# Kernel optimization log

Measured on AMD Instinct MI355X. Metric: run time of the kernel, lower is better.

Reference implementation:

```python
import jax, jax.numpy as jnp
import numpy as np

B, N, V, C, H, W = 4, 2048, 4, 64, 32, 32
D, K, OUT, HEADS = 128, 64, 256, 4
IMG_W, IMG_H = W * 14.0, H * 14.0
EPS_NORM = 1e-12


def setup_inputs() -> dict:
    key = jax.random.key(0)
    ks = iter(jax.random.split(key, 64))
    nk = lambda: next(ks)
    rn = lambda shape, s=1.0: jax.random.normal(nk(), shape, jnp.float32) * s
    eye4 = jnp.broadcast_to(jnp.eye(4, dtype=jnp.float32), (B, V, 4, 4))
    Kbase = jnp.array([[400.0, 0.0, IMG_W / 2], [0.0, 400.0, IMG_H / 2], [0.0, 0.0, 1.0]], jnp.float32)
    inp = {
        'gaussians': rn((B, N, 14)),
        'visual_feats': rn((B * V, C, H, W)),
        'extrinsics': eye4 + rn((B, V, 4, 4), 0.1),
        'intrinsics': jnp.broadcast_to(Kbase, (B, V, 3, 3)) + rn((B, V, 3, 3), 0.5),
        'offsets': rn((B, N, 2), 0.05),
        'pg_w': rn((D, 14), 0.1), 'pg_b': jnp.zeros((D,)), 'pg_ln_g': jnp.ones((D,)), 'pg_ln_b': jnp.zeros((D,)),
        'pv_w': rn((D, C), 0.1), 'pv_b': jnp.zeros((D,)), 'pv_ln_g': jnp.ones((D,)), 'pv_ln_b': jnp.zeros((D,)),
        'attn_ipw': rn((2, 3 * D, D), 0.05), 'attn_ipb': jnp.zeros((2, 3 * D)),
        'attn_ow': rn((2, D, D), 0.05), 'attn_ob': jnp.zeros((2, D)),
        'dca_ln_g': jnp.ones((2, D)), 'dca_ln_b': jnp.zeros((2, D)),
        'gate_w': rn((D, 2 * D), 0.05), 'gate_b': jnp.zeros((D,)),
        'router_w1': rn((D, 2 * D), 0.05), 'router_b1': jnp.zeros((D,)),
        'router_ln_g': jnp.ones((D,)), 'router_ln_b': jnp.zeros((D,)),
        'router_w2': rn((3, D), 0.01), 'router_b2': jnp.array([-3.0, -3.0, 2.0], jnp.float32),
        'vlad_cent': jnp.clip(rn((3, K, D), 0.01), -2.0, 2.0),
        'vlad_cw': rn((3, K, D), 0.05), 'vlad_cb': jnp.zeros((3, K)),
        'bn_w': rn((3, OUT, K * D), 0.01), 'bn_b': jnp.zeros((3, OUT)),
        'bn_ln_g': jnp.ones((3, OUT)), 'bn_ln_b': jnp.zeros((3, OUT)),
    }
    return inp


def _ln(x, g, b, eps=1e-5):
    m = x.mean(-1, keepdims=True)
    v = ((x - m) ** 2).mean(-1, keepdims=True)
    return (x - m) * jax.lax.rsqrt(v + eps) * g + b


def _l2n(x, axis):
    return x / jnp.maximum(jnp.linalg.norm(x, axis=axis, keepdims=True), EPS_NORM)


def _bilinear(fm, grid):
    # fm: [BV,H,W,C]; grid: [BV,N,2] in [-1,1]; align_corners=False, zero padding
    x = (grid[..., 0] + 1.0) * 0.5 * W - 0.5
    y = (grid[..., 1] + 1.0) * 0.5 * H - 0.5
    x0, y0 = jnp.floor(x), jnp.floor(y)
    fmf = fm.reshape(fm.shape[0], H * W, C)
    out = jnp.zeros((fm.shape[0], grid.shape[1], C), jnp.float32)
    for xi in (x0, x0 + 1.0):
        for yi in (y0, y0 + 1.0):
            wgt = (1.0 - jnp.abs(x - xi)) * (1.0 - jnp.abs(y - yi))
            valid = (xi >= 0) & (xi < W) & (yi >= 0) & (yi < H)
            idx = (jnp.clip(yi, 0, H - 1) * W + jnp.clip(xi, 0, W - 1)).astype(jnp.int32)
            v = jnp.take_along_axis(fmf, idx[..., None], axis=1)
            out = out + v * (wgt * valid.astype(jnp.float32))[..., None]
    return out


def _mha(q, k, v, ipw, ipb, ow, ob):
    Wq, Wk, Wv = jnp.split(ipw, 3, axis=0)
    bq, bk, bv = jnp.split(ipb, 3)
    dh = D // HEADS
    sh = lambda x, Wt, b: (x @ Wt.T + b).reshape(x.shape[0], x.shape[1], HEADS, dh)
    qh, kh, vh = sh(q, Wq, bq), sh(k, Wk, bk), sh(v, Wv, bv)
    att = jax.nn.softmax(jnp.einsum('bqhd,bkhd->bhqk', qh, kh) * (1.0 / np.sqrt(dh)), axis=-1)
    o = jnp.einsum('bhqk,bkhd->bqhd', att, vh).reshape(q.shape[0], q.shape[1], D)
    return o @ ow.T + ob


def _netvlad(x, cent, cw, cb):
    xn = _l2n(x, 2)                                   # [B,N,D]
    a = jax.nn.softmax(xn @ cw.T + cb, axis=-1)       # [B,N,K]
    # sum_n a[bnk]*(x[bnd]-c[kd]) without materializing [B,N,K,D]
    vlad = jnp.einsum('bnk,bnd->bkd', a, xn) - a.sum(1)[..., None] * cent
    vlad = _l2n(vlad, 2).reshape(x.shape[0], -1)
    return _l2n(vlad, 1)


def reference(gaussians, visual_feats, extrinsics, intrinsics, offsets,
              pg_w, pg_b, pg_ln_g, pg_ln_b, pv_w, pv_b, pv_ln_g, pv_ln_b,
              attn_ipw, attn_ipb, attn_ow, attn_ob, dca_ln_g, dca_ln_b,
              gate_w, gate_b, router_w1, router_b1, router_ln_g, router_ln_b,
              router_w2, router_b2, vlad_cent, vlad_cw, vlad_cb,
              bn_w, bn_b, bn_ln_g, bn_ln_b):
    # ---- DynamicProjectionLayer (vectorized over views) ----
    ph = jnp.concatenate([gaussians[:, :, :3], jnp.ones((B, N, 1), jnp.float32)], axis=2)
    cam = jnp.einsum('bvij,bnj->bvni', extrinsics, ph)          # [B,V,N,4]
    p2h = jnp.einsum('bvij,bvnj->bvni', intrinsics, cam[..., :3])
    depth = jnp.maximum(p2h[..., 2:3], 1e-6)
    p2 = p2h[..., :2] / depth
    grid = 2.0 * p2 / jnp.array([IMG_W, IMG_H], jnp.float32) - 1.0 + offsets[:, None]
    fm = visual_feats.reshape(B, V, C, H, W).transpose(0, 1, 3, 4, 2).reshape(B * V, H, W, C)
    sampled = _bilinear(fm, grid.reshape(B * V, N, 2)).reshape(B, V, N, C)
    valid = ((depth[..., 0] > 0.1) & (grid[..., 0] >= -1) & (grid[..., 0] <= 1)
             & (grid[..., 1] >= -1) & (grid[..., 1] <= 1)).astype(jnp.float32)[..., None]
    vfeat = (sampled * valid).sum(1) / (valid.sum(1) + 1e-8)     # [B,N,C]
    # ---- GaussianEncoder ----
    g_emb = jax.nn.relu(_ln(gaussians @ pg_w.T + pg_b, pg_ln_g, pg_ln_b))
    v_emb = jax.nn.relu(_ln(vfeat @ pv_w.T + pv_b, pv_ln_g, pv_ln_b))
    f_g2v = _ln(g_emb + _mha(g_emb, v_emb, v_emb, attn_ipw[0], attn_ipb[0], attn_ow[0], attn_ob[0]),
                dca_ln_g[0], dca_ln_b[0])
    f_v2g = _ln(v_emb + _mha(v_emb, g_emb, g_emb, attn_ipw[1], attn_ipb[1], attn_ow[1], attn_ob[1]),
                dca_ln_g[1], dca_ln_b[1])
    gate = jax.nn.sigmoid(jnp.concatenate([f_g2v, f_v2g], -1) @ gate_w.T + gate_b)
    fused = f_g2v * gate + f_v2g * (1.0 - gate)
    ri = jnp.concatenate([g_emb.mean(1), v_emb.mean(1)], -1)
    rw = jax.nn.softmax(jax.nn.relu(_ln(ri @ router_w1.T + router_b1, router_ln_g, router_ln_b))
                        @ router_w2.T + router_b2, axis=-1)
    descs = []
    for i, feat in enumerate((g_emb, v_emb, fused)):
        d = _netvlad(feat, vlad_cent[i], vlad_cw[i], vlad_cb[i])
        d = _ln(d @ bn_w[i].T + bn_b[i], bn_ln_g[i], bn_ln_b[i])
        descs.append(_l2n(d, 1))
    final = rw[:, 0:1] * descs[0] + rw[:, 1:2] * descs[1] + rw[:, 2:3] * descs[2]
    return _l2n(final, 1), rw
```

## Files before the change

kernel.cpp:

```cpp
#include <hip/hip_runtime.h>
#include <math.h>

typedef float f32x4 __attribute__((ext_vector_type(4)));
typedef short s16x8 __attribute__((ext_vector_type(8)));

#define DEV static __device__ __forceinline__

DEV float wsum(float v){
  #pragma unroll
  for(int m=1;m<64;m<<=1) v += __shfl_xor(v,m);
  return v;
}
template<int NW>
DEV float bsum(float v, float* s){
  v = wsum(v);
  int w = threadIdx.x>>6;
  if((threadIdx.x&63)==0) s[w]=v;
  __syncthreads();
  float r = 0.f;
  #pragma unroll
  for(int i=0;i<NW;++i) r += s[i];
  __syncthreads();
  return r;
}
DEV float xexp2(float x){
#if __has_builtin(__builtin_amdgcn_exp2f)
  return __builtin_amdgcn_exp2f(x);
#else
  return exp2f(x);
#endif
}
DEV unsigned pkbf(float lo, float hi){
  unsigned r;
  asm("v_cvt_pk_bf16_f32 %0, %1, %2" : "=v"(r) : "v"(lo), "v"(hi));
  return r;
}
DEV unsigned short bf16c(float v){ return (unsigned short)(pkbf(v, 0.f) & 0xffffu); }
DEV float ubf_lo(unsigned u){ unsigned b=(u&0xffffu)<<16; return __builtin_bit_cast(float,b); }
DEV float ubf_hi(unsigned u){ unsigned b=(u>>16)<<16;    return __builtin_bit_cast(float,b); }
union FR { unsigned u[4]; s16x8 v; uint4 q; };

DEV f32x4 MF(s16x8 a, s16x8 b, f32x4 c){
  return __builtin_amdgcn_mfma_f32_16x16x32_bf16(a, b, c, 0,0,0);
}

DEV void gl_lds16(const void* g, void* l){
  __builtin_amdgcn_global_load_lds(
    (const __attribute__((address_space(1))) void*)g,
    (__attribute__((address_space(3))) void*)l, 16, 0, 0);
}

__global__ __launch_bounds__(256) void k_trfm(const float* __restrict__ vf, float* __restrict__ fmT){
  int hc = blockIdx.x, bv = blockIdx.y, t = threadIdx.x;
  __shared__ float ts[64][65];
  const float* src = vf + (size_t)bv*65536 + hc*64;
  int c = t>>2, q = t&3;
  #pragma unroll
  for(int i=0;i<4;++i){
    float4 v4 = *(const float4*)(src + (size_t)c*1024 + q*16 + i*4);
    ts[c][q*16+i*4+0]=v4.x; ts[c][q*16+i*4+1]=v4.y;
    ts[c][q*16+i*4+2]=v4.z; ts[c][q*16+i*4+3]=v4.w;
  }
  __syncthreads();
  int hw = t>>2;
  float* dst = fmT + ((size_t)bv*1024 + hc*64 + hw)*64 + q*16;
  #pragma unroll
  for(int i=0;i<4;++i){
    int cb = q*16 + i*4;
    float4 o4;
    o4.x = ts[cb+0][hw]; o4.y = ts[cb+1][hw]; o4.z = ts[cb+2][hw]; o4.w = ts[cb+3][hw];
    *(float4*)(dst + i*4) = o4;
  }
}

__global__ __launch_bounds__(256) void k_proj(const float* __restrict__ gs, const float* __restrict__ fmT,
                       const float* __restrict__ E, const float* __restrict__ Kin,
                       const float* __restrict__ off, float* __restrict__ vfeat){
  int bn = blockIdx.x*4 + (threadIdx.x>>6); int b = bn>>11; int c = threadIdx.x&63;
  const float* g = gs + (size_t)bn*14;
  float px = g[0], py = g[1], pz = g[2];
  float ox = off[bn*2+0], oy = off[bn*2+1];
  float acc = 0.f, vsum = 0.f;
  for(int v=0; v<4; ++v){
    const float* e = E + ((b*4+v)*16);
    float cx = e[0]*px + e[1]*py + e[2]*pz + e[3];
    float cy = e[4]*px + e[5]*py + e[6]*pz + e[7];
    float cz = e[8]*px + e[9]*py + e[10]*pz + e[11];
    const float* kk = Kin + ((b*4+v)*9);
    float ux = kk[0]*cx + kk[1]*cy + kk[2]*cz;
    float uy = kk[3]*cx + kk[4]*cy + kk[5]*cz;
    float uz = kk[6]*cx + kk[7]*cy + kk[8]*cz;
    float dep = fmaxf(uz, 1e-6f);
    float gx = 2.f*(ux/dep)*(1.f/448.f) - 1.f + ox;
    float gy = 2.f*(uy/dep)*(1.f/448.f) - 1.f + oy;
    float valid = (uz > 0.1f && gx >= -1.f && gx <= 1.f && gy >= -1.f && gy <= 1.f) ? 1.f : 0.f;
    float x = (gx+1.f)*16.f - 0.5f;
    float y = (gy+1.f)*16.f - 0.5f;
    float x0 = floorf(x), y0 = floorf(y);
    const float* fbase = fmT + (size_t)(b*4+v)*65536 + c;
    float sv = 0.f;
    #pragma unroll
    for(int t=0;t<4;++t){
      float xi = x0 + (float)(t&1), yi = y0 + (float)(t>>1);
      float wgt = (1.f - fabsf(x-xi))*(1.f - fabsf(y-yi));
      bool vt = (xi>=0.f && xi<32.f && yi>=0.f && yi<32.f);
      int xc = (int)fminf(fmaxf(xi,0.f),31.f);
      int yc = (int)fminf(fmaxf(yi,0.f),31.f);
      float smp = fbase[(yc*32+xc)*64];
      sv += vt ? wgt*smp : 0.f;
    }
    acc += valid * sv;
    vsum += valid;
  }
  vfeat[(size_t)bn*64 + c] = acc / (vsum + 1e-8f);
}

__global__ void k_embed(const float* __restrict__ gs, const float* __restrict__ vfeat,
   const float* __restrict__ pg_w, const float* __restrict__ pg_b,
   const float* __restrict__ pg_g, const float* __restrict__ pg_bb,
   const float* __restrict__ pv_w, const float* __restrict__ pv_b,
   const float* __restrict__ pv_g, const float* __restrict__ pv_bb,
   float* __restrict__ gemb, float* __restrict__ vemb,
   unsigned short* __restrict__ gembb, unsigned short* __restrict__ vembb){
  __shared__ float xs[64]; __shared__ float gsr[14]; __shared__ float red[2];
  int row = blockIdx.x; int d = threadIdx.x;
  if(d<14) gsr[d] = gs[(size_t)row*14+d];
  if(d<64) xs[d] = vfeat[(size_t)row*64+d];
  __syncthreads();
  float a = pg_b[d];
  #pragma unroll
  for(int j=0;j<14;++j) a += gsr[j]*pg_w[d*14+j];
  float mu = bsum<2>(a, red)*(1.f/128.f);
  float df = a-mu;
  float var = bsum<2>(df*df, red)*(1.f/128.f);
  float y = fmaxf(df*rsqrtf(var+1e-5f)*pg_g[d] + pg_bb[d], 0.f);
  gemb[(size_t)row*128+d] = y;
  gembb[(size_t)row*128+d] = bf16c(y);
  float av = pv_b[d];
  #pragma unroll
  for(int j=0;j<64;++j) av += xs[j]*pv_w[d*64+j];
  mu = bsum<2>(av, red)*(1.f/128.f);
  df = av-mu;
  var = bsum<2>(df*df, red)*(1.f/128.f);
  y = fmaxf(df*rsqrtf(var+1e-5f)*pv_g[d] + pv_bb[d], 0.f);
  vemb[(size_t)row*128+d] = y;
  vembb[(size_t)row*128+d] = bf16c(y);
}

__global__ void k_wprep(const float* __restrict__ ipw, const float* __restrict__ ow,
                        const float* __restrict__ gw, const float* __restrict__ cw,
                        unsigned short* __restrict__ WB){
  int i = blockIdx.x*256 + threadIdx.x;
  if(i >= 188416) return;
  float v;
  if(i < 98304)       v = ipw[i];
  else if(i < 131072) v = ow[i-98304];
  else if(i < 163840) v = gw[i-131072];
  else                v = cw[i-163840];
  WB[i] = bf16c(v);
}

__global__ __launch_bounds__(256) void k_qkv(const unsigned short* __restrict__ GEb,
    const unsigned short* __restrict__ VEb, const unsigned short* __restrict__ WB,
    const float* __restrict__ ipb, unsigned* __restrict__ QKVu, float qsc){
  int mt = blockIdx.x, y = blockIdx.y;
  int m = y/6, j6 = y%6, kind = j6>>1, n0 = (j6&1)*64;
  const unsigned short* A = (kind==0) ? (m?VEb:GEb) : (m?GEb:VEb);
  const unsigned short* W = WB + m*49152 + kind*16384;
  const float* bias = ipb + m*384 + kind*128;
  unsigned* outb = QKVu + (size_t)m*1572864 + (size_t)kind*524288;
  float scale = (kind==0)? qsc : 1.f;
  int m0 = mt*64;
  int wid=threadIdx.x>>6, lane=threadIdx.x&63, lr=lane&15, lg=lane>>4;
  const unsigned short* ap = A + (size_t)(m0+wid*16+lr)*128 + lg*8;
  f32x4 acc[4] = {{0,0,0,0},{0,0,0,0},{0,0,0,0},{0,0,0,0}};
  #pragma unroll
  for(int ks=0; ks<128; ks+=32){
    FR af; af.v = *(const s16x8*)(ap + ks);
    #pragma unroll
    for(int nt=0; nt<4; ++nt){
      FR bf; bf.v = *(const s16x8*)(W + (size_t)(n0+nt*16+lr)*128 + ks + lg*8);
      acc[nt] = MF(af.v, bf.v, acc[nt]);
    }
  }
  __shared__ float xs[64][65];
  #pragma unroll
  for(int nt=0; nt<4; ++nt){
    float bv = bias[n0+nt*16+lr];
    #pragma unroll
    for(int r=0;r<4;++r) xs[wid*16+lg*4+r][nt*16+lr] = (acc[nt][r]+bv)*scale;
  }
  __syncthreads();
  if(kind<2){
    int i = threadIdx.x>>2, s = threadIdx.x&3;
    int gr = m0 + i, b = gr>>11, nn = gr&2047;
    int j0 = n0 + s*16, h = j0>>5, d0 = j0&31;
    unsigned w[8];
    #pragma unroll
    for(int p=0;p<8;++p) w[p] = pkbf(xs[i][s*16+2*p], xs[i][s*16+2*p+1]);
    unsigned* dst = outb + ((size_t)(b*4+h)*2048+nn)*16 + (d0>>1);
    uint4 u0; u0.x=w[0];u0.y=w[1];u0.z=w[2];u0.w=w[3];
    uint4 u1; u1.x=w[4];u1.y=w[5];u1.z=w[6];u1.w=w[7];
    *(uint4*)dst = u0; *(uint4*)(dst+4) = u1;
  } else {
    int c = threadIdx.x>>2, rs = threadIdx.x&3;
    int j = n0 + c, h = j>>5, d = j&31;
    int b = m0>>11, nn0 = m0&2047;
    unsigned w[8];
    #pragma unroll
    for(int p=0;p<8;++p) w[p] = pkbf(xs[rs*16+2*p][c], xs[rs*16+2*p+1][c]);
    unsigned* dst = outb + (size_t)(b*4+h)*32768 + (size_t)d*1024 + ((nn0+rs*16)>>1);
    uint4 u0; u0.x=w[0];u0.y=w[1];u0.z=w[2];u0.w=w[3];
    uint4 u1; u1.x=w[4];u1.y=w[5];u1.z=w[6];u1.w=w[7];
    *(uint4*)dst = u0; *(uint4*)(dst+4) = u1;
  }
}

__global__ __launch_bounds__(256) void k_flash(const unsigned short* __restrict__ QKV,
    unsigned* __restrict__ OPARTw, float* __restrict__ LSUM){
  int qt = blockIdx.x, h = blockIdx.y, z = blockIdx.z;
  int mb = z&7, split = z>>3;
  int m = mb>>2, b = mb&3;
  const unsigned short* base = QKV + (size_t)m*3145728;
  const unsigned short* qp = base + (size_t)(b*4+h)*65536;
  const unsigned short* kp = qp + 1048576;
  const unsigned short* vp = qp + 2097152;
  int tid=threadIdx.x, wid=tid>>6, lane=tid&63, lr=lane&15, lg=lane>>4;
  __shared__ unsigned short KT[2][2048];
  __shared__ unsigned short VT[2][2048];
  __shared__ unsigned Ps[4][16][33];
  int q0 = qt*64 + wid*16;
  int kbase = split*1024;
  FR qf; qf.v = *(const s16x8*)(qp + (size_t)(q0+lr)*32 + lg*8);
  const f32x4 zz = {0.f,0.f,0.f,0.f};
  f32x4 o0g = zz, o1g = zz;
  float lrun = 0.f;
  unsigned* prow = &Ps[wid][lr][0];
  int kr = wid*16 + (lane>>2);
  int kscol = (((lane&3)<<3) ^ (((lane>>3)&3)<<3));
  const unsigned short* ksrc0 = kp + (size_t)(kbase + kr)*32 + kscol;
  int vrow = wid*8 + (lane>>3);
  int vscol = 8*((lane&7) ^ (lane>>3));
  const unsigned short* vsrc0 = vp + (size_t)vrow*2048 + kbase + vscol;
  int kkey = ((lr>>1)&3)<<3;
  int ko = lr*32 + ((lg*8) ^ kkey);
  int sw = (lr&7)*8;
  int vo0 = lr*64 + ((lg*8) ^ sw);
  int vo2 = lr*64 + ((32+lg*8) ^ sw);
  gl_lds16(ksrc0, &KT[0][wid*512]);
  gl_lds16(vsrc0, &VT[0][wid*512]);
  __syncthreads();
  int buf = 0;
  for(int t=0; t<16; ++t){
    int tn = (t+1)&15;
    gl_lds16(ksrc0 + (size_t)tn*2048, &KT[buf^1][wid*512]);
    gl_lds16(vsrc0 + tn*64,           &VT[buf^1][wid*512]);
    const unsigned short* Ktb = &KT[buf][0];
    const unsigned short* Vtb = &VT[buf][0];
    FR k0,k1,k2,k3;
    k0.v = *(const s16x8*)(Ktb + ko);
    k1.v = *(const s16x8*)(Ktb +  512 + ko);
    k2.v = *(const s16x8*)(Ktb + 1024 + ko);
    k3.v = *(const s16x8*)(Ktb + 1536 + ko);
    f32x4 s0 = MF(k0.v, qf.v, zz);
    f32x4 s1 = MF(k1.v, qf.v, zz);
    f32x4 s2 = MF(k2.v, qf.v, zz);
    f32x4 s3 = MF(k3.v, qf.v, zz);
    float p0[4],p1[4],p2[4],p3[4]; float ps=0.f;
    #pragma unroll
    for(int r=0;r<4;++r){
      p0[r]=xexp2(s0[r]); p1[r]=xexp2(s1[r]);
      p2[r]=xexp2(s2[r]); p3[r]=xexp2(s3[r]);
      ps += p0[r]+p1[r]+p2[r]+p3[r];
    }
    lrun += ps;
    asm volatile("" ::: "memory");
    prow[   lg*2+0]=pkbf(p0[0],p0[1]); prow[   lg*2+1]=pkbf(p0[2],p0[3]);
    prow[ 8+lg*2+0]=pkbf(p1[0],p1[1]); prow[ 8+lg*2+1]=pkbf(p1[2],p1[3]);
    prow[16+lg*2+0]=pkbf(p2[0],p2[1]); prow[16+lg*2+1]=pkbf(p2[2],p2[3]);
    prow[24+lg*2+0]=pkbf(p3[0],p3[1]); prow[24+lg*2+1]=pkbf(p3[2],p3[3]);
    asm volatile("" ::: "memory");
    FR pf0, pf1;
    #pragma unroll
    for(int i=0;i<4;++i){ pf0.u[i]=prow[lg*4+i]; pf1.u[i]=prow[16+lg*4+i]; }
    FR v0,v1,v2,v3;
    v0.v = *(const s16x8*)(Vtb + vo0);
    v1.v = *(const s16x8*)(Vtb + 1024 + vo0);
    v2.v = *(const s16x8*)(Vtb + vo2);
    v3.v = *(const s16x8*)(Vtb + 1024 + vo2);
    o0g = MF(v0.v, pf0.v, o0g);
    o1g = MF(v1.v, pf0.v, o1g);
    o0g = MF(v2.v, pf1.v, o0g);
    o1g = MF(v3.v, pf1.v, o1g);
    __syncthreads();
    buf ^= 1;
  }
  lrun += __shfl_xor(lrun,16); lrun += __shfl_xor(lrun,32);
  unsigned w00=pkbf(o0g[0],o0g[1]), w01=pkbf(o0g[2],o0g[3]);
  unsigned w10=pkbf(o1g[0],o1g[1]), w11=pkbf(o1g[2],o1g[3]);
  unsigned* op = OPARTw + ((size_t)(split*2+m)*8192 + (size_t)(b*2048+q0+lr))*64 + h*16 + lg*2;
  op[0]=w00; op[1]=w01; op[8]=w10; op[9]=w11;
  if(lg==0) LSUM[((size_t)(split*2+m)*16 + b*4+h)*2048 + q0+lr] = lrun;
}

__global__ __launch_bounds__(256) void k_oproj(const unsigned* __restrict__ OPARTw,
    const float* __restrict__ LSUM,
    const unsigned short* __restrict__ WB, const float* __restrict__ ob,
    const float* __restrict__ GE, const float* __restrict__ VE,
    const float* __restrict__ dg, const float* __restrict__ db,
    float* __restrict__ CC, unsigned short* __restrict__ CCb){
  int mt = blockIdx.x, m = blockIdx.y;
  int m0 = mt*64;
  const unsigned short* W = WB + 98304 + m*16384;
  const float* bias = ob + m*128;
  const float* R = m ? VE : GE;
  const float* gamma = dg + m*128;
  const float* beta  = db + m*128;
  int wid=threadIdx.x>>6, lane=threadIdx.x&63, lr=lane&15, lg=lane>>4;
  int gr = m0 + wid*16 + lr;
  int b2 = gr>>11, nn = gr&2047;
  float invh[4];
  #pragma unroll
  for(int h=0;h<4;++h){
    float l0 = LSUM[((size_t)(m*16) + b2*4+h)*2048 + nn];
    float l1 = LSUM[((size_t)((2+m)*16) + b2*4+h)*2048 + nn];
    invh[h] = 1.f/(l0+l1);
  }
  const unsigned* a0 = OPARTw + ((size_t)m*8192 + gr)*64 + lg*4;
  const unsigned* a1 = OPARTw + ((size_t)(2+m)*8192 + gr)*64 + lg*4;
  f32x4 acc[8] = {};
  #pragma unroll
  for(int ks=0; ks<4; ++ks){
    uint4 u0 = *(const uint4*)(a0 + ks*16);
    uint4 u1 = *(const uint4*)(a1 + ks*16);
    float sc = invh[ks];
    FR af;
    af.u[0] = pkbf((ubf_lo(u0.x)+ubf_lo(u1.x))*sc, (ubf_hi(u0.x)+ubf_hi(u1.x))*sc);
    af.u[1] = pkbf((ubf_lo(u0.y)+ubf_lo(u1.y))*sc, (ubf_hi(u0.y)+ubf_hi(u1.y))*sc);
    af.u[2] = pkbf((ubf_lo(u0.z)+ubf_lo(u1.z))*sc, (ubf_hi(u0.z)+ubf_hi(u1.z))*sc);
    af.u[3] = pkbf((ubf_lo(u0.w)+ubf_lo(u1.w))*sc, (ubf_hi(u0.w)+ubf_hi(u1.w))*sc);
    #pragma unroll
    for(int nt=0; nt<8; ++nt){
      FR bf; bf.v = *(const s16x8*)(W + (size_t)(nt*16+lr)*128 + ks*32 + lg*8);
      acc[nt] = MF(af.v, bf.v, acc[nt]);
    }
  }
  __shared__ float xs[64][129];
  __shared__ float mus[64], rss[64];
  #pragma unroll
  for(int nt=0; nt<8; ++nt){
    float bv = bias[nt*16+lr];
    #pragma unroll
    for(int r=0;r<4;++r){
      int row = wid*16+lg*4+r;
      xs[row][nt*16+lr] = acc[nt][r] + bv + R[(size_t)(m0+row)*128 + nt*16+lr];
    }
  }
  __syncthreads();
  if(threadIdx.x < 64){
    int row = threadIdx.x;
    float s=0.f, s2=0.f;
    #pragma unroll 8
    for(int c=0;c<128;++c){ float x = xs[row][c]; s += x; s2 += x*x; }
    float mu = s*(1.f/128.f);
    float var = fmaxf(s2*(1.f/128.f) - mu*mu, 0.f);
    mus[row] = mu; rss[row] = rsqrtf(var + 1e-5f);
  }
  __syncthreads();
  int row = threadIdx.x>>2, cs = (threadIdx.x&3)*32;
  float mu = mus[row], rs = rss[row];
  size_t obase = (size_t)(m0+row)*256 + m*128;
  #pragma unroll 8
  for(int c=cs;c<cs+32;++c){
    float y = (xs[row][c]-mu)*rs*gamma[c] + beta[c];
    CC [obase + c] = y;
    CCb[obase + c] = bf16c(y);
  }
}

__global__ __launch_bounds__(256) void k_gatef(const unsigned short* __restrict__ CCb,
    const unsigned short* __restrict__ WB, const float* __restrict__ gate_b,
    const float* __restrict__ CC, float* __restrict__ FU){
  int mt = blockIdx.x;
  int m0 = mt*64;
  const unsigned short* W = WB + 131072;
  int wid=threadIdx.x>>6, lane=threadIdx.x&63, lr=lane&15, lg=lane>>4;
  const unsigned short* ap = CCb + (size_t)(m0+wid*16+lr)*256 + lg*8;
  f32x4 acc[8] = {};
  #pragma unroll
  for(int ks=0; ks<256; ks+=32){
    FR af; af.v = *(const s16x8*)(ap + ks);
    #pragma unroll
    for(int nt=0; nt<8; ++nt){
      FR bf; bf.v = *(const s16x8*)(W + (size_t)(nt*16+lr)*256 + ks + lg*8);
      acc[nt] = MF(af.v, bf.v, acc[nt]);
    }
  }
  #pragma unroll
  for(int nt=0; nt<8; ++nt){
    int col = nt*16+lr;
    float bv = gate_b[col];
    #pragma unroll
    for(int r=0;r<4;++r){
      int row = m0 + wid*16+lg*4+r;
      float gv = 1.f/(1.f+__expf(-(acc[nt][r]+bv)));
      FU[(size_t)row*128 + col] = CC[(size_t)row*256 + col]*gv
                                + CC[(size_t)row*256 + 128 + col]*(1.f-gv);
    }
  }
}

__global__ __launch_bounds__(256) void k_rpart(const float* __restrict__ gemb, const float* __restrict__ vemb,
                        float* __restrict__ part){
  int blk = blockIdx.x;
  int b = blk>>7, ch = blk&127, t = threadIdx.x;
  const float* src = (t<128)? gemb : vemb;
  int d = t&127;
  float s=0.f;
  int n0 = ch*16;
  for(int n=0;n<16;++n) s += src[((size_t)(b*2048+n0+n))*128 + d];
  part[(size_t)blk*256 + t] = s;
}
__global__ void k_router(const float* __restrict__ part, const float* __restrict__ w1,
     const float* __restrict__ b1, const float* __restrict__ lg, const float* __restrict__ lb,
     const float* __restrict__ w2, const float* __restrict__ b2,
     float* __restrict__ rw, float* __restrict__ outrw){
  __shared__ float ri[256]; __shared__ float red[2];
  int b = blockIdx.x, t = threadIdx.x;
  for(int j=t; j<256; j+=128){
    float s=0.f;
    for(int c=0;c<128;++c) s += part[(size_t)(b*128+c)*256 + j];
    ri[j] = s*(1.f/2048.f);
  }
  __syncthreads();
  float a = b1[t];
  for(int j=0;j<256;++j) a += ri[j]*w1[t*256+j];
  float mu = bsum<2>(a,red)*(1.f/128.f);
  float df = a-mu;
  float var = bsum<2>(df*df,red)*(1.f/128.f);
  float hv = fmaxf(df*rsqrtf(var+1e-5f)*lg[t]+lb[t], 0.f);
  float l0 = bsum<2>(hv*w2[t],red);
  float l1 = bsum<2>(hv*w2[128+t],red);
  float l2 = bsum<2>(hv*w2[256+t],red);
  if(t==0){
    l0+=b2[0]; l1+=b2[1]; l2+=b2[2];
    float mx = fmaxf(l0,fmaxf(l1,l2));
    float e0=__expf(l0-mx), e1=__expf(l1-mx), e2=__expf(l2-mx);
    float s=e0+e1+e2;
    rw[b*3+0]=e0/s; rw[b*3+1]=e1/s; rw[b*3+2]=e2/s;
    outrw[b*3+0]=e0/s; outrw[b*3+1]=e1/s; outrw[b*3+2]=e2/s;
  }
}

__global__ __launch_bounds__(256) void k_vlad1(
      const float* __restrict__ GE, const float* __restrict__ VE, const float* __restrict__ FU,
      const unsigned short* __restrict__ WBcw, const float* __restrict__ cbp,
      float* __restrict__ p0, float* __restrict__ p1, float* __restrict__ p2,
      float* __restrict__ asump){
  int ch = blockIdx.x, b = blockIdx.y, z = blockIdx.z;
  const float* feat = (z==0)?GE:((z==1)?VE:FU);
  const unsigned short* cwb = WBcw + z*8192;
  const float* cb = cbp + z*64;
  float* part = (z==0)?p0:((z==1)?p1:p2);
  float* asu = asump + z*8192;
  int t = threadIdx.x;
  __shared__ unsigned xnbu[64*36];
  __shared__ unsigned short xnbT[128*72];
  __shared__ unsigned abTu[64*36];
  int nbase = b*2048 + ch*64;
  {
    int r = t>>2, q = t&3;
    const float* frow = feat + (size_t)(nbase + r)*128 + q*32;
    float v[32]; float ssq = 0.f;
    #pragma unroll
    for(int i=0;i<8;++i){
      float4 f4 = *(const float4*)(frow + i*4);
      v[i*4+0]=f4.x; v[i*4+1]=f4.y; v[i*4+2]=f4.z; v[i*4+3]=f4.w;
      ssq += f4.x*f4.x+f4.y*f4.y+f4.z*f4.z+f4.w*f4.w;
    }
    ssq += __shfl_xor(ssq,1); ssq += __shfl_xor(ssq,2);
    float inv = 1.f/fmaxf(sqrtf(ssq),1e-12f);
    #pragma unroll
    for(int i=0;i<16;++i)
      xnbu[r*36 + q*8 + i] = pkbf(v[2*i]*inv, v[2*i+1]*inv);
    #pragma unroll
    for(int j=0;j<32;++j)
      xnbT[(q*32+j)*72 + r] = bf16c(v[j]*inv);
  }
  __syncthreads();
  int w = t>>6, lane = t&63, lr = lane&15, lg = lane>>4;
  {
    f32x4 acc[4] = {};
    #pragma unroll
    for(int ks=0; ks<4; ++ks){
      FR af; af.q = *(const uint4*)&xnbu[(w*16+lr)*36 + ks*16 + lg*4];
      #pragma unroll
      for(int nt=0; nt<4; ++nt){
        FR bf; bf.v = *(const s16x8*)(cwb + (size_t)(nt*16+lr)*128 + ks*32 + lg*8);
        acc[nt] = MF(af.v, bf.v, acc[nt]);
      }
    }
    float p[4][4]; float srow[4] = {0.f,0.f,0.f,0.f};
    #pragma unroll
    for(int nt=0;nt<4;++nt){
      float cbv = cb[nt*16+lr];
      #pragma unroll
      for(int rr=0;rr<4;++rr){
        p[nt][rr] = __expf(acc[nt][rr] + cbv);
        srow[rr] += p[nt][rr];
      }
    }
    #pragma unroll
    for(int rr=0;rr<4;++rr){
      float s = srow[rr];
      s += __shfl_xor(s,1); s += __shfl_xor(s,2); s += __shfl_xor(s,4); s += __shfl_xor(s,8);
      srow[rr] = 1.f/s;
    }
    #pragma unroll
    for(int nt=0;nt<4;++nt){
      int k = nt*16+lr;
      abTu[k*36 + w*8 + lg*2 + 0] = pkbf(p[nt][0]*srow[0], p[nt][1]*srow[1]);
      abTu[k*36 + w*8 + lg*2 + 1] = pkbf(p[nt][2]*srow[2], p[nt][3]*srow[3]);
    }
  }
  __syncthreads();
  {
    f32x4 acc[8] = {};
    #pragma unroll
    for(int ns=0; ns<2; ++ns){
      FR af; af.q = *(const uint4*)&abTu[(w*16+lr)*36 + ns*16 + lg*4];
      #pragma unroll
      for(int nt=0; nt<8; ++nt){
        FR bf; bf.v = *(const s16x8*)&xnbT[(nt*16+lr)*72 + ns*32 + lg*8];
        acc[nt] = MF(af.v, bf.v, acc[nt]);
      }
    }
    size_t pb = ((size_t)(b*32+ch)*64);
    #pragma unroll
    for(int nt=0; nt<8; ++nt){
      #pragma unroll
      for(int rr=0; rr<4; ++rr){
        int k = w*16+lg*4+rr;
        part[(pb + k)*128 + nt*16+lr] = acc[nt][rr];
      }
    }
  }
  if(t<64){
    float s = 0.f;
    #pragma unroll
    for(int i=0;i<32;++i){
      unsigned u = abTu[t*36+i];
      s += ubf_lo(u) + ubf_hi(u);
    }
    asu[((size_t)(b*32+ch))*64 + t] = s;
  }
}

__global__ void k_vagg2(
      const float* __restrict__ p0, const float* __restrict__ p1, const float* __restrict__ p2,
      const float* __restrict__ asump, const float* __restrict__ cent, float* __restrict__ vlad3){
  int k = blockIdx.x, b = blockIdx.y, z = blockIdx.z;
  const float* part = (z==0)?p0:((z==1)?p1:p2);
  const float* asu = asump + z*8192;
  const float* centp = cent + (size_t)z*8192;
  float* vlad = vlad3 + z*32768;
  int t = threadIdx.x;
  __shared__ float red[2];
  float v = 0.f;
  const float* pp = part + (((size_t)b*32)*64 + k)*128 + t;
  for(int ch=0; ch<32; ++ch) v += pp[(size_t)ch*8192];
  float as = 0.f;
  const float* ap = asu + (size_t)b*2048 + k;
  for(int ch=0; ch<32; ++ch) as += ap[(size_t)ch*64];
  v -= as * centp[(size_t)k*128 + t];
  float ssq = bsum<2>(v*v, red);
  float inv = 1.f/fmaxf(sqrtf(ssq),1e-12f);
  vlad[((size_t)b*64+k)*128+t] = v*inv;
}

__global__ __launch_bounds__(256) void k_desc(const float* __restrict__ vlad3,
      const float* __restrict__ bnw, const float* __restrict__ bnb, float* __restrict__ DT){
  int jg = blockIdx.x, b = blockIdx.y, z = blockIdx.z;
  const float* vlad = vlad3 + z*32768;
  const float* bw = bnw + (size_t)z*2097152;
  const float* bb = bnb + z*256;
  float* dtmp = DT + z*1024;
  int t = threadIdx.x;
  __shared__ float fl[8192]; __shared__ float red[4];
  const float4* src = (const float4*)(vlad + (size_t)b*8192);
  float4* fl4 = (float4*)fl;
  float ssq = 0.f;
  #pragma unroll
  for(int i=0;i<8;++i){
    float4 vv = src[t + i*256]; fl4[t+i*256]=vv;
    ssq += vv.x*vv.x+vv.y*vv.y+vv.z*vv.z+vv.w*vv.w;
  }
  ssq = bsum<4>(ssq, red);
  float inv = 1.f/fmaxf(sqrtf(ssq),1e-12f);
  for(int jj=0;jj<4;++jj){
    int j = jg*4 + jj;
    const float4* wp = (const float4*)(bw + (size_t)j*8192);
    float s = 0.f;
    #pragma unroll
    for(int i=0;i<8;++i){
      int f = t + i*256;
      float4 w4 = wp[f]; float4 x4 = fl4[f];
      s += w4.x*x4.x+w4.y*x4.y+w4.z*x4.z+w4.w*x4.w;
    }
    s = bsum<4>(s, red);
    if(t==0) dtmp[(size_t)b*256 + j] = s*inv + bb[j];
  }
}

__global__ void k_final(const float* __restrict__ dtmp, const float* __restrict__ lg,
      const float* __restrict__ lb, const float* __restrict__ rw, float* __restrict__ outp){
  __shared__ float red[4];
  int b = blockIdx.x, t = threadIdx.x;
  float acc = 0.f;
  for(int i=0;i<3;++i){
    float x = dtmp[(size_t)(i*4+b)*256 + t];
    float mu = bsum<4>(x,red)*(1.f/256.f);
    float df = x-mu;
    float var = bsum<4>(df*df,red)*(1.f/256.f);
    float y = df*rsqrtf(var+1e-5f)*lg[i*256+t]+lb[i*256+t];
    float n2 = bsum<4>(y*y,red);
    y = y / fmaxf(sqrtf(n2),1e-12f);
    acc += rw[b*3+i]*y;
  }
  float n2 = bsum<4>(acc*acc,red);
  outp[(size_t)b*256+t] = acc/fmaxf(sqrtf(n2),1e-12f);
}

extern "C" void kernel_launch(void* const* d_in, const int* in_sizes, int n_in,
                              void* d_out, int out_size, void* d_ws, size_t ws_size,
                              hipStream_t stream){
  const float* gaussians=(const float*)d_in[0];
  const float* visual=(const float*)d_in[1];
  const float* extr=(const float*)d_in[2];
  const float* intr=(const float*)d_in[3];
  const float* offs=(const float*)d_in[4];
  const float* pg_w=(const float*)d_in[5];
  const float* pg_b=(const float*)d_in[6];
  const float* pg_g=(const float*)d_in[7];
  const float* pg_bb=(const float*)d_in[8];
  const float* pv_w=(const float*)d_in[9];
  const float* pv_b=(const float*)d_in[10];
  const float* pv_g=(const float*)d_in[11];
  const float* pv_bb=(const float*)d_in[12];
  const float* ipw=(const float*)d_in[13];
  const float* ipb=(const float*)d_in[14];
  const float* ow=(const float*)d_in[15];
  const float* ob=(const float*)d_in[16];
  const float* dg=(const float*)d_in[17];
  const float* db=(const float*)d_in[18];
  const float* gate_w=(const float*)d_in[19];
  const float* gate_b=(const float*)d_in[20];
  const float* rw1=(const float*)d_in[21];
  const float* rb1=(const float*)d_in[22];
  const float* rlg=(const float*)d_in[23];
  const float* rlb=(const float*)d_in[24];
  const float* rw2=(const float*)d_in[25];
  const float* rb2=(const float*)d_in[26];
  const float* cent=(const float*)d_in[27];
  const float* cw=(const float*)d_in[28];
  const float* cb=(const float*)d_in[29];
  const float* bnw=(const float*)d_in[30];
  const float* bnb=(const float*)d_in[31];
  const float* blg=(const float*)d_in[32];
  const float* blb=(const float*)d_in[33];
  float* outp=(float*)d_out;
  float* ws=(float*)d_ws;

  float* FMT = ws + 0;
  float* VF  = ws + 1048576;
  float* GE  = ws + 1572864;
  float* VE  = ws + 2621440;
  unsigned short* GEb = (unsigned short*)(ws + 3670016);
  unsigned short* VEb = (unsigned short*)(ws + 4194304);
  unsigned* QKVu = (unsigned*)(ws + 4718592);
  float* CC  = ws + 4718592;
  unsigned short* CCb = (unsigned short*)(ws + 6815744);
  unsigned* OPARTw = (unsigned*)(ws + 7864320);
  float* FU  = ws + 8912896;
  unsigned short* WB = (unsigned short*)(ws + 9961472);
  float* DT  = ws + 10072064;
  float* RW  = ws + 10075136;
  float* VLAD3 = ws + 10075152;
  float* PART2 = ws + 10173456;
  float* ASUMP3 = ws + 11222032;
  float* LSUM  = ws + 11246608;
  float* RP    = ws + 11246608;
  float* PART0 = ws + 3670016;
  float* PART1 = ws + 7864320;
  const unsigned short* QKVh = (const unsigned short*)QKVu;

  k_trfm<<<dim3(16,16),256,0,stream>>>(visual, FMT);
  k_proj<<<2048,256,0,stream>>>(gaussians, FMT, extr, intr, offs, VF);
  k_embed<<<8192,128,0,stream>>>(gaussians, VF, pg_w,pg_b,pg_g,pg_bb,
                                 pv_w,pv_b,pv_g,pv_bb, GE, VE, GEb, VEb);
  k_rpart<<<512,256,0,stream>>>(GE, VE, RP);
  k_router<<<4,128,0,stream>>>(RP, rw1,rb1,rlg,rlb,rw2,rb2, RW, outp+1024);
  k_wprep<<<736,256,0,stream>>>(ipw, ow, gate_w, cw, WB);

  const float qsc = 1.4426950408889634f * 0.17677669529663687f;
  k_qkv<<<dim3(128,12),256,0,stream>>>(GEb, VEb, WB, ipb, QKVu, qsc);
  k_flash<<<dim3(32,4,16),256,0,stream>>>(QKVh, OPARTw, LSUM);
  k_oproj<<<dim3(128,2),256,0,stream>>>(OPARTw, LSUM, WB, ob, GE, VE, dg, db, CC, CCb);
  k_gatef<<<128,256,0,stream>>>(CCb, WB, gate_b, CC, FU);
  k_vlad1<<<dim3(32,4,3),256,0,stream>>>(GE, VE, FU, WB+163840, cb,
                                         PART0, PART1, PART2, ASUMP3);
  k_vagg2<<<dim3(64,4,3),128,0,stream>>>(PART0,PART1,PART2, ASUMP3, cent, VLAD3);
  k_desc<<<dim3(64,4,3),256,0,stream>>>(VLAD3, bnw, bnb, DT);
  k_final<<<4,256,0,stream>>>(DT, blg, blb, RW, outp);
}
```

Measured before the change: 197.5 us.

## Drop feature-map transpose kernel and pass P via lane shuffles in flash

Removes the k_trfm transpose launch, so k_proj samples the channel-major visual features directly, with 64 lanes reading strided addresses (stride 1024 floats) instead of contiguous channel rows. In k_flash, the probability tile is redistributed across lanes with __shfl instead of going through an LDS staging buffer, which removes the shared array and its write/read round trip. The gather in k_proj becomes uncoalesced, which may cost more than the launch and transpose it saves, and the shuffles add cross-lane instructions.

Result: slower. 212.0 us (+7.4%).

```diff
diff --git a/kernel.cpp b/kernel.cpp
--- a/kernel.cpp
+++ b/kernel.cpp
@@ -50,30 +50,7 @@
     (__attribute__((address_space(3))) void*)l, 16, 0, 0);
 }
 
-__global__ __launch_bounds__(256) void k_trfm(const float* __restrict__ vf, float* __restrict__ fmT){
-  int hc = blockIdx.x, bv = blockIdx.y, t = threadIdx.x;
-  __shared__ float ts[64][65];
-  const float* src = vf + (size_t)bv*65536 + hc*64;
-  int c = t>>2, q = t&3;
-  #pragma unroll
-  for(int i=0;i<4;++i){
-    float4 v4 = *(const float4*)(src + (size_t)c*1024 + q*16 + i*4);
-    ts[c][q*16+i*4+0]=v4.x; ts[c][q*16+i*4+1]=v4.y;
-    ts[c][q*16+i*4+2]=v4.z; ts[c][q*16+i*4+3]=v4.w;
-  }
-  __syncthreads();
-  int hw = t>>2;
-  float* dst = fmT + ((size_t)bv*1024 + hc*64 + hw)*64 + q*16;
-  #pragma unroll
-  for(int i=0;i<4;++i){
-    int cb = q*16 + i*4;
-    float4 o4;
-    o4.x = ts[cb+0][hw]; o4.y = ts[cb+1][hw]; o4.z = ts[cb+2][hw]; o4.w = ts[cb+3][hw];
-    *(float4*)(dst + i*4) = o4;
-  }
-}
-
-__global__ __launch_bounds__(256) void k_proj(const float* __restrict__ gs, const float* __restrict__ fmT,
+__global__ __launch_bounds__(256) void k_proj(const float* __restrict__ gs, const float* __restrict__ vf,
                        const float* __restrict__ E, const float* __restrict__ Kin,
                        const float* __restrict__ off, float* __restrict__ vfeat){
   int bn = blockIdx.x*4 + (threadIdx.x>>6); int b = bn>>11; int c = threadIdx.x&63;
@@ -97,7 +74,7 @@
     float x = (gx+1.f)*16.f - 0.5f;
     float y = (gy+1.f)*16.f - 0.5f;
     float x0 = floorf(x), y0 = floorf(y);
-    const float* fbase = fmT + (size_t)(b*4+v)*65536 + c;
+    const float* fbase = vf + (size_t)((b*4+v)*64 + c)*1024;
     float sv = 0.f;
     #pragma unroll
     for(int t=0;t<4;++t){
@@ -106,7 +83,7 @@
       bool vt = (xi>=0.f && xi<32.f && yi>=0.f && yi<32.f);
       int xc = (int)fminf(fmaxf(xi,0.f),31.f);
       int yc = (int)fminf(fmaxf(yi,0.f),31.f);
-      float smp = fbase[(yc*32+xc)*64];
+      float smp = fbase[yc*32+xc];
       sv += vt ? wgt*smp : 0.f;
     }
     acc += valid * sv;
@@ -228,14 +205,12 @@
   int tid=threadIdx.x, wid=tid>>6, lane=tid&63, lr=lane&15, lg=lane>>4;
   __shared__ unsigned short KT[2][2048];
   __shared__ unsigned short VT[2][2048];
-  __shared__ unsigned Ps[4][16][33];
   int q0 = qt*64 + wid*16;
   int kbase = split*1024;
   FR qf; qf.v = *(const s16x8*)(qp + (size_t)(q0+lr)*32 + lg*8);
   const f32x4 zz = {0.f,0.f,0.f,0.f};
   f32x4 o0g = zz, o1g = zz;
   float lrun = 0.f;
-  unsigned* prow = &Ps[wid][lr][0];
   int kr = wid*16 + (lane>>2);
   int kscol = (((lane&3)<<3) ^ (((lane>>3)&3)<<3));
   const unsigned short* ksrc0 = kp + (size_t)(kbase + kr)*32 + kscol;
@@ -247,6 +222,9 @@
   int sw = (lr&7)*8;
   int vo0 = lr*64 + ((lg*8) ^ sw);
   int vo2 = lr*64 + ((32+lg*8) ^ sw);
+  int ls0 = lr + (((2*lg)  )&3)*16;
+  int ls1 = lr + (((2*lg)+1)&3)*16;
+  bool lowg = (lg<2);
   gl_lds16(ksrc0, &KT[0][wid*512]);
   gl_lds16(vsrc0, &VT[0][wid*512]);
   __syncthreads();
@@ -274,15 +252,23 @@
       ps += p0[r]+p1[r]+p2[r]+p3[r];
     }
     lrun += ps;
-    asm volatile("" ::: "memory");
-    prow[   lg*2+0]=pkbf(p0[0],p0[1]); prow[   lg*2+1]=pkbf(p0[2],p0[3]);
-    prow[ 8+lg*2+0]=pkbf(p1[0],p1[1]); prow[ 8+lg*2+1]=pkbf(p1[2],p1[3]);
-    prow[16+lg*2+0]=pkbf(p2[0],p2[1]); prow[16+lg*2+1]=pkbf(p2[2],p2[3]);
-    prow[24+lg*2+0]=pkbf(p3[0],p3[1]); prow[24+lg*2+1]=pkbf(p3[2],p3[3]);
-    asm volatile("" ::: "memory");
+    int a0=pkbf(p0[0],p0[1]), a1=pkbf(p0[2],p0[3]);
+    int b0=pkbf(p1[0],p1[1]), b1=pkbf(p1[2],p1[3]);
+    int c0=pkbf(p2[0],p2[1]), c1=pkbf(p2[2],p2[3]);
+    int d0=pkbf(p3[0],p3[1]), d1=pkbf(p3[2],p3[3]);
+    int ra0=__shfl(a0,ls0), ra1=__shfl(a1,ls0), ra2=__shfl(a0,ls1), ra3=__shfl(a1,ls1);
+    int rb0=__shfl(b0,ls0), rb1=__shfl(b1,ls0), rb2=__shfl(b0,ls1), rb3=__shfl(b1,ls1);
+    int rc0=__shfl(c0,ls0), rc1=__shfl(c1,ls0), rc2=__shfl(c0,ls1), rc3=__shfl(c1,ls1);
+    int rd0=__shfl(d0,ls0), rd1=__shfl(d1,ls0), rd2=__shfl(d0,ls1), rd3=__shfl(d1,ls1);
     FR pf0, pf1;
-    #pragma unroll
-    for(int i=0;i<4;++i){ pf0.u[i]=prow[lg*4+i]; pf1.u[i]=prow[16+lg*4+i]; }
+    pf0.u[0] = lowg ? (unsigned)ra0 : (unsigned)rb0;
+    pf0.u[1] = lowg ? (unsigned)ra1 : (unsigned)rb1;
+    pf0.u[2] = lowg ? (unsigned)ra2 : (unsigned)rb2;
+    pf0.u[3] = lowg ? (unsigned)ra3 : (unsigned)rb3;
+    pf1.u[0] = lowg ? (unsigned)rc0 : (unsigned)rd0;
+    pf1.u[1] = lowg ? (unsigned)rc1 : (unsigned)rd1;
+    pf1.u[2] = lowg ? (unsigned)rc2 : (unsigned)rd2;
+    pf1.u[3] = lowg ? (unsigned)rc3 : (unsigned)rd3;
     FR v0,v1,v2,v3;
     v0.v = *(const s16x8*)(Vtb + vo0);
     v1.v = *(const s16x8*)(Vtb + 1024 + vo0);
@@ -671,7 +657,6 @@
   float* outp=(float*)d_out;
   float* ws=(float*)d_ws;
 
-  float* FMT = ws + 0;
   float* VF  = ws + 1048576;
   float* GE  = ws + 1572864;
   float* VE  = ws + 2621440;
@@ -694,8 +679,7 @@
   float* PART1 = ws + 7864320;
   const unsigned short* QKVh = (const unsigned short*)QKVu;
 
-  k_trfm<<<dim3(16,16),256,0,stream>>>(visual, FMT);
-  k_proj<<<2048,256,0,stream>>>(gaussians, FMT, extr, intr, offs, VF);
+  k_proj<<<2048,256,0,stream>>>(gaussians, visual, extr, intr, offs, VF);
   k_embed<<<8192,128,0,stream>>>(gaussians, VF, pg_w,pg_b,pg_g,pg_bb,
                                  pv_w,pv_b,pv_g,pv_bb, GE, VE, GEb, VEb);
   k_rpart<<<512,256,0,stream>>>(GE, VE, RP);
```
